# Performance work log

Measured on AMD Instinct MI355X. Metric: run time of the kernel, lower is better.

## Reference

```python
import jax, jax.numpy as jnp
import numpy as np

EPS = 1e-5
HEADS = 8
DIM_KEY = 128
K = 16           # num_experts_per_head
NUM_KEYS = 256   # sqrt(num_experts)


def setup_inputs() -> dict:
    key = jax.random.key(0)
    ks = jax.random.split(key, 5)
    B, T, D = 1, 1024, 1024
    x = jax.random.normal(ks[0], (B, T, D), dtype=jnp.float32)
    norm_w = jnp.ones((D,), dtype=jnp.float32)
    wq = jax.random.normal(ks[1], (D, DIM_KEY * HEADS * 2), dtype=jnp.float32) * 0.02
    keys = jax.random.normal(ks[2], (HEADS, NUM_KEYS, 2, DIM_KEY), dtype=jnp.float32) * 0.02
    expert_down = jax.random.normal(ks[3], (NUM_KEYS * NUM_KEYS, D), dtype=jnp.float32) * 0.02
    expert_up = jax.random.normal(ks[4], (NUM_KEYS * NUM_KEYS, D), dtype=jnp.float32) * 0.02
    return {"x": x, "norm_w": norm_w, "wq": wq, "keys": keys,
            "expert_down": expert_down, "expert_up": expert_up}


def reference(x, norm_w, wq, keys, expert_down, expert_up):
    B, T, D = x.shape
    # RMSNorm
    inv = jax.lax.rsqrt(jnp.mean(x * x, axis=-1, keepdims=True) + EPS)
    x_norm = x * inv * norm_w                                   # [B,T,D]
    # queries -> [B,T,H,2,dk]
    q = (x_norm @ wq).reshape(B, T, HEADS, 2, DIM_KEY)
    # similarity with product keys: sim[p] for each of the two sub-key sets
    sim = jnp.einsum('bthpd,hkpd->pbthk', q, keys)              # [2,B,T,H,NUM_KEYS]
    s1, i1 = jax.lax.top_k(sim[0], K)                           # [B,T,H,K]
    s2, i2 = jax.lax.top_k(sim[1], K)
    # cartesian product of the two top-k sets
    all_idx = (i1[..., :, None] * NUM_KEYS + i2[..., None, :]).reshape(B, T, HEADS, K * K)
    all_scores = (s1[..., :, None] + s2[..., None, :]).reshape(B, T, HEADS, K * K)
    final_scores, pk = jax.lax.top_k(all_scores, K)             # [B,T,H,K]
    final_idx = jnp.take_along_axis(all_idx, pk, axis=-1)       # [B,T,H,K]
    # gather expert vectors
    wd = expert_down[final_idx]                                 # [B,T,H,K,D]
    wu = expert_up[final_idx]                                   # [B,T,H,K,D]
    hidden = jnp.einsum('btd,bthkd->bthk', x_norm, wd)
    hidden = jax.nn.gelu(hidden, approximate=False)             # torch nn.GELU default = erf
    hidden = hidden * jax.nn.relu(final_scores)
    out = jnp.einsum('bthk,bthkd->btd', hidden, wu)             # [B,T,D]
    return out
```

## Files before the change

kernel.cpp:

```cpp
#include <hip/hip_runtime.h>
#include <hip/hip_bf16.h>
#include <math.h>

#define T_TOK   1024
#define D_MODEL 1024
#define H_HEADS 8
#define DKEY    128
#define NKEYS   256
#define TOPK    16
#define TPB     4

__device__ __forceinline__ float dot4(float4 a, float4 b){
  return a.x*b.x + a.y*b.y + a.z*b.z + a.w*b.w;
}

__global__ __launch_bounds__(256) void k_rmsnorm(const float* __restrict__ x,
                                                 const float* __restrict__ nw,
                                                 float* __restrict__ xn)
{
  const int t = blockIdx.x, tid = threadIdx.x;
  const float4 v = *(const float4*)(x + (size_t)t*D_MODEL + tid*4);
  float ss = dot4(v, v);
  #pragma unroll
  for (int m = 1; m < 64; m <<= 1) ss += __shfl_xor(ss, m, 64);
  __shared__ float part[4];
  const int lane = tid & 63, wid = tid >> 6;
  if (lane == 0) part[wid] = ss;
  __syncthreads();
  const float tot = part[0] + part[1] + part[2] + part[3];
  const float inv = rsqrtf(tot * (1.0f/(float)D_MODEL) + 1e-5f);
  const float4 w = *(const float4*)(nw + tid*4);
  float4 o;
  o.x = v.x*inv*w.x; o.y = v.y*inv*w.y; o.z = v.z*inv*w.z; o.w = v.w*inv*w.w;
  *(float4*)(xn + (size_t)t*D_MODEL + tid*4) = o;
}

#define TBM 64
#define TBN 64
#define TBK 16
__global__ __launch_bounds__(256) void k_qgemm(const float* __restrict__ A,
                                               const float* __restrict__ B,
                                               float* __restrict__ C)
{
  const int N = 2048, Kd = 1024;
  __shared__ float As[TBK][TBM+4];
  __shared__ float Bs[TBK][TBN+4];
  const int tid = threadIdx.x;
  const int row0 = blockIdx.y * TBM, col0 = blockIdx.x * TBN;
  const int ar = tid >> 2,  ac = (tid & 3) * 4;
  const int br = tid >> 4,  bc = (tid & 15) * 4;
  const int ty = tid >> 4,  tx = tid & 15;
  float acc[4][4] = {{0}};
  for (int k0 = 0; k0 < Kd; k0 += TBK){
    const float4 a = *(const float4*)(A + (size_t)(row0+ar)*Kd + k0 + ac);
    const float4 b = *(const float4*)(B + (size_t)(k0+br)*N + col0 + bc);
    As[ac+0][ar] = a.x; As[ac+1][ar] = a.y; As[ac+2][ar] = a.z; As[ac+3][ar] = a.w;
    *(float4*)&Bs[br][bc] = b;
    __syncthreads();
    #pragma unroll
    for (int kk = 0; kk < TBK; kk++){
      const float4 av = *(const float4*)&As[kk][ty*4];
      const float4 bv = *(const float4*)&Bs[kk][tx*4];
      acc[0][0] += av.x*bv.x; acc[0][1] += av.x*bv.y; acc[0][2] += av.x*bv.z; acc[0][3] += av.x*bv.w;
      acc[1][0] += av.y*bv.x; acc[1][1] += av.y*bv.y; acc[1][2] += av.y*bv.z; acc[1][3] += av.y*bv.w;
      acc[2][0] += av.z*bv.x; acc[2][1] += av.z*bv.y; acc[2][2] += av.z*bv.z; acc[2][3] += av.z*bv.w;
      acc[3][0] += av.w*bv.x; acc[3][1] += av.w*bv.y; acc[3][2] += av.w*bv.z; acc[3][3] += av.w*bv.w;
    }
    __syncthreads();
  }
  #pragma unroll
  for (int i = 0; i < 4; i++){
    float4 o; o.x = acc[i][0]; o.y = acc[i][1]; o.z = acc[i][2]; o.w = acc[i][3];
    *(float4*)(C + (size_t)(row0 + ty*4 + i)*N + col0 + tx*4) = o;
  }
}

__global__ __launch_bounds__(256) void k_simgemm(const float* __restrict__ Q,
                                                 const float* __restrict__ keys,
                                                 float* __restrict__ sims)
{
  const int hp = blockIdx.z;
  const int t0 = blockIdx.y * 64, kb0 = blockIdx.x * 64;
  const float* A = Q + (size_t)t0*2048 + (hp>>1)*256 + (hp&1)*128;
  const float* B = keys + ((size_t)((hp>>1)*NKEYS + kb0)*2 + (hp&1)) * DKEY;
  __shared__ float As[TBK][64+4];
  __shared__ float Bs[TBK][64+4];
  const int tid = threadIdx.x;
  const int ar = tid >> 2, ac = (tid & 3) * 4;
  const int ty = tid >> 4, tx = tid & 15;
  float acc[4][4] = {{0}};
  for (int kd = 0; kd < DKEY; kd += TBK){
    const float4 a = *(const float4*)(A + (size_t)ar*2048 + kd + ac);
    const float4 b = *(const float4*)(B + (size_t)ar*256  + kd + ac);
    As[ac+0][ar] = a.x; As[ac+1][ar] = a.y; As[ac+2][ar] = a.z; As[ac+3][ar] = a.w;
    Bs[ac+0][ar] = b.x; Bs[ac+1][ar] = b.y; Bs[ac+2][ar] = b.z; Bs[ac+3][ar] = b.w;
    __syncthreads();
    #pragma unroll
    for (int kk = 0; kk < TBK; kk++){
      const float4 av = *(const float4*)&As[kk][ty*4];
      const float4 bv = *(const float4*)&Bs[kk][tx*4];
      acc[0][0] += av.x*bv.x; acc[0][1] += av.x*bv.y; acc[0][2] += av.x*bv.z; acc[0][3] += av.x*bv.w;
      acc[1][0] += av.y*bv.x; acc[1][1] += av.y*bv.y; acc[1][2] += av.y*bv.z; acc[1][3] += av.y*bv.w;
      acc[2][0] += av.z*bv.x; acc[2][1] += av.z*bv.y; acc[2][2] += av.z*bv.z; acc[2][3] += av.z*bv.w;
      acc[3][0] += av.w*bv.x; acc[3][1] += av.w*bv.y; acc[3][2] += av.w*bv.z; acc[3][3] += av.w*bv.w;
    }
    __syncthreads();
  }
  float* Cb = sims + (size_t)t0*4096 + hp*256 + kb0;
  #pragma unroll
  for (int i = 0; i < 4; i++){
    float4 o; o.x = acc[i][0]; o.y = acc[i][1]; o.z = acc[i][2]; o.w = acc[i][3];
    *(float4*)(Cb + (size_t)(ty*4 + i)*4096 + tx*4) = o;
  }
}

__device__ __forceinline__ void wave_top16(float v[4], int lane, float* tvO, int* tiO)
{
  for (int r = 0; r < 16; r++){
    float bv = v[0]; int bj = 0;
    #pragma unroll
    for (int j = 1; j < 4; j++) if (v[j] > bv){ bv = v[j]; bj = j; }
    int bi = lane*4 + bj;
    #pragma unroll
    for (int m = 1; m < 64; m <<= 1){
      const float ov = __shfl_xor(bv, m, 64);
      const int   oi = __shfl_xor(bi, m, 64);
      if (ov > bv || (ov == bv && oi < bi)){ bv = ov; bi = oi; }
    }
    if (lane == 0){ tvO[r] = bv; tiO[r] = bi; }
    if ((bi >> 2) == lane) v[bi & 3] = -INFINITY;
  }
}

__global__ __launch_bounds__(256) void k_topk(const float* __restrict__ sims,
                                              int* __restrict__ fidxO,
                                              float* __restrict__ gateO)
{
  const int h  = blockIdx.x;
  const int t0 = blockIdx.y * TPB;
  const int tid = threadIdx.x;
  const int w = tid >> 6, lane = tid & 63;
  const int t = t0 + w;
  __shared__ float tv[TPB][2][TOPK];
  __shared__ int   ti[TPB][2][TOPK];

  float v0[4], v1[4];
  {
    const float4 a = *(const float4*)(sims + (size_t)t*4096 + (h*2+0)*256 + lane*4);
    const float4 b = *(const float4*)(sims + (size_t)t*4096 + (h*2+1)*256 + lane*4);
    v0[0]=a.x; v0[1]=a.y; v0[2]=a.z; v0[3]=a.w;
    v1[0]=b.x; v1[1]=b.y; v1[2]=b.z; v1[3]=b.w;
  }
  wave_top16(v0, lane, &tv[w][0][0], &ti[w][0][0]);
  wave_top16(v1, lane, &tv[w][1][0], &ti[w][1][0]);

  float cv[4];
  const int i0 = lane >> 2;
  #pragma unroll
  for (int j = 0; j < 4; j++)
    cv[j] = tv[w][0][i0] + tv[w][1][4*(lane & 3) + j];

  const size_t obase = (size_t)((t)*H_HEADS + h) * TOPK;
  for (int r = 0; r < 16; r++){
    float bv = cv[0]; int bj = 0;
    #pragma unroll
    for (int j = 1; j < 4; j++) if (cv[j] > bv){ bv = cv[j]; bj = j; }
    int bc = lane*4 + bj;
    #pragma unroll
    for (int m = 1; m < 64; m <<= 1){
      const float ov = __shfl_xor(bv, m, 64);
      const int   oc = __shfl_xor(bc, m, 64);
      if (ov > bv || (ov == bv && oc < bc)){ bv = ov; bc = oc; }
    }
    if (lane == 0){
      fidxO[obase + r] = ti[w][0][bc >> 4] * NKEYS + ti[w][1][bc & 15];
      gateO[obase + r] = bv > 0.0f ? bv : 0.0f;
    }
    if ((bc >> 2) == lane) cv[bc & 3] = -INFINITY;
  }
}

__global__ __launch_bounds__(256) void k_expert(const float* __restrict__ xn,
                                                const float* __restrict__ ed,
                                                const float* __restrict__ eu,
                                                const int* __restrict__ fidx,
                                                const float* __restrict__ gate,
                                                float* __restrict__ out)
{
  const int t = blockIdx.x, tid = threadIdx.x;
  const int lane = tid & 63, wid = tid >> 6;
  const float4 xv = *(const float4*)(xn + (size_t)t*D_MODEL + tid*4);
  float4 acc = {0.f, 0.f, 0.f, 0.f};
  __shared__ int   sidx[TOPK];
  __shared__ float wred[TOPK][4];
  __shared__ float coeff[TOPK];

  for (int h = 0; h < H_HEADS; ++h){
    const int base = (t*H_HEADS + h)*TOPK;
    if (tid < TOPK) sidx[tid] = fidx[base + tid];
    __syncthreads();

    {
      float4 wv[TOPK];
      #pragma unroll
      for (int k = 0; k < TOPK; k++)
        wv[k] = *(const float4*)(ed + (size_t)sidx[k]*D_MODEL + tid*4);
      #pragma unroll
      for (int k = 0; k < TOPK; k++){
        float p = dot4(xv, wv[k]);
        #pragma unroll
        for (int m = 1; m < 64; m <<= 1) p += __shfl_xor(p, m, 64);
        if (lane == 0) wred[k][wid] = p;
      }
    }
    __syncthreads();
    if (tid < TOPK){
      const float hsum = wred[tid][0] + wred[tid][1] + wred[tid][2] + wred[tid][3];
      const float g = 0.5f * hsum * (1.0f + erff(hsum * 0.70710678118654752440f));
      coeff[tid] = g * gate[base + tid];
    }
    __syncthreads();

    {
      float4 wv[TOPK];
      #pragma unroll
      for (int k = 0; k < TOPK; k++)
        wv[k] = *(const float4*)(eu + (size_t)sidx[k]*D_MODEL + tid*4);
      #pragma unroll
      for (int k = 0; k < TOPK; k++){
        const float c = coeff[k];
        acc.x += c*wv[k].x; acc.y += c*wv[k].y; acc.z += c*wv[k].z; acc.w += c*wv[k].w;
      }
    }
    __syncthreads();
  }
  *(float4*)(out + (size_t)t*D_MODEL + tid*4) = acc;
}

extern "C" void kernel_launch(void* const* d_in, const int* in_sizes, int n_in,
                              void* d_out, int out_size, void* d_ws, size_t ws_size,
                              hipStream_t stream)
{
  const float* x      = (const float*)d_in[0];
  const float* norm_w = (const float*)d_in[1];
  const float* wq     = (const float*)d_in[2];
  const float* keys   = (const float*)d_in[3];
  const float* ed     = (const float*)d_in[4];
  const float* eu     = (const float*)d_in[5];
  float* out = (float*)d_out;

  float* xn   = (float*)d_ws;
  float* q    = xn + (size_t)T_TOK * D_MODEL;
  int*   fidx = (int*)(q + (size_t)T_TOK * 2048);
  float* gate = (float*)(fidx + (size_t)T_TOK * H_HEADS * TOPK);
  float* sims = gate + (size_t)T_TOK * H_HEADS * TOPK;

  k_rmsnorm<<<T_TOK, 256, 0, stream>>>(x, norm_w, xn);
  k_qgemm<<<dim3(2048/TBN, 1024/TBM), 256, 0, stream>>>(xn, wq, q);
  k_simgemm<<<dim3(NKEYS/64, T_TOK/64, 16), 256, 0, stream>>>(q, keys, sims);
  k_topk<<<dim3(H_HEADS, T_TOK/TPB), 256, 0, stream>>>(sims, fidx, gate);
  k_expert<<<T_TOK, 256, 0, stream>>>(xn, ed, eu, fidx, gate, out);
}
```

Before: 321.0 us.

## Split expert stage into parallel down-projection and sync-free up-projection kernels

The fused per-token expert kernel, which looped over heads with several block barriers, is split into two kernels. The first launches one block per (token, head), with each wave computing four full-row dot products for the down projection, GELU and gate coefficients. The second accumulates all 128 up-projection rows per token with no per-head barriers, keeping 8 gathers in flight per step. This raises parallelism and memory-level concurrency for the gather-bound work, at the cost of an extra launch and a coefficient round-trip through global memory, which reuses the sims buffer.

```diff
diff --git a/kernel.cpp b/kernel.cpp
--- a/kernel.cpp
+++ b/kernel.cpp
@@ -180,59 +180,73 @@
   }
 }
 
-__global__ __launch_bounds__(256) void k_expert(const float* __restrict__ xn,
-                                                const float* __restrict__ ed,
-                                                const float* __restrict__ eu,
-                                                const int* __restrict__ fidx,
-                                                const float* __restrict__ gate,
-                                                float* __restrict__ out)
+__global__ __launch_bounds__(256) void k_peer_down(const float* __restrict__ xn,
+                                                   const float* __restrict__ ed,
+                                                   const int* __restrict__ fidx,
+                                                   const float* __restrict__ gate,
+                                                   float* __restrict__ coeff)
+{
+  const int b = blockIdx.x;
+  const int t = b >> 3;
+  const int tid = threadIdx.x, w = tid >> 6, lane = tid & 63;
+  const int base = b * TOPK;
+
+  float4 xv[4];
+  #pragma unroll
+  for (int j = 0; j < 4; j++)
+    xv[j] = *(const float4*)(xn + (size_t)t*D_MODEL + j*256 + lane*4);
+
+  int e[4];
+  #pragma unroll
+  for (int r = 0; r < 4; r++) e[r] = fidx[base + w*4 + r];
+
+  float4 wv[4][4];
+  #pragma unroll
+  for (int r = 0; r < 4; r++)
+    #pragma unroll
+    for (int j = 0; j < 4; j++)
+      wv[r][j] = *(const float4*)(ed + (size_t)e[r]*D_MODEL + j*256 + lane*4);
+
+  float s[4];
+  #pragma unroll
+  for (int r = 0; r < 4; r++){
+    float p = dot4(wv[r][0], xv[0]) + dot4(wv[r][1], xv[1])
+            + dot4(wv[r][2], xv[2]) + dot4(wv[r][3], xv[3]);
+    #pragma unroll
+    for (int m = 1; m < 64; m <<= 1) p += __shfl_xor(p, m, 64);
+    s[r] = p;
+  }
+  if (lane < 4){
+    const float hs = (lane == 0) ? s[0] : (lane == 1) ? s[1] : (lane == 2) ? s[2] : s[3];
+    const float g = 0.5f * hs * (1.0f + erff(hs * 0.70710678118654752440f));
+    coeff[base + w*4 + lane] = g * gate[base + w*4 + lane];
+  }
+}
+
+__global__ __launch_bounds__(256) void k_peer_up(const float* __restrict__ eu,
+                                                 const int* __restrict__ fidx,
+                                                 const float* __restrict__ coeff,
+                                                 float* __restrict__ out)
 {
   const int t = blockIdx.x, tid = threadIdx.x;
-  const int lane = tid & 63, wid = tid >> 6;
-  const float4 xv = *(const float4*)(xn + (size_t)t*D_MODEL + tid*4);
+  __shared__ int   sidx[H_HEADS*TOPK];
+  __shared__ float sc[H_HEADS*TOPK];
+  if (tid < H_HEADS*TOPK){
+    sidx[tid] = fidx[(size_t)t*H_HEADS*TOPK + tid];
+    sc[tid]   = coeff[(size_t)t*H_HEADS*TOPK + tid];
+  }
+  __syncthreads();
   float4 acc = {0.f, 0.f, 0.f, 0.f};
-  __shared__ int   sidx[TOPK];
-  __shared__ float wred[TOPK][4];
-  __shared__ float coeff[TOPK];
-
-  for (int h = 0; h < H_HEADS; ++h){
-    const int base = (t*H_HEADS + h)*TOPK;
-    if (tid < TOPK) sidx[tid] = fidx[base + tid];
-    __syncthreads();
-
-    {
-      float4 wv[TOPK];
-      #pragma unroll
-      for (int k = 0; k < TOPK; k++)
-        wv[k] = *(const float4*)(ed + (size_t)sidx[k]*D_MODEL + tid*4);
-      #pragma unroll
-      for (int k = 0; k < TOPK; k++){
-        float p = dot4(xv, wv[k]);
-        #pragma unroll
-        for (int m = 1; m < 64; m <<= 1) p += __shfl_xor(p, m, 64);
-        if (lane == 0) wred[k][wid] = p;
-      }
-    }
-    __syncthreads();
-    if (tid < TOPK){
-      const float hsum = wred[tid][0] + wred[tid][1] + wred[tid][2] + wred[tid][3];
-      const float g = 0.5f * hsum * (1.0f + erff(hsum * 0.70710678118654752440f));
-      coeff[tid] = g * gate[base + tid];
-    }
-    __syncthreads();
-
-    {
-      float4 wv[TOPK];
-      #pragma unroll
-      for (int k = 0; k < TOPK; k++)
-        wv[k] = *(const float4*)(eu + (size_t)sidx[k]*D_MODEL + tid*4);
-      #pragma unroll
-      for (int k = 0; k < TOPK; k++){
-        const float c = coeff[k];
-        acc.x += c*wv[k].x; acc.y += c*wv[k].y; acc.z += c*wv[k].z; acc.w += c*wv[k].w;
-      }
-    }
-    __syncthreads();
+  for (int j = 0; j < H_HEADS*TOPK; j += 8){
+    float4 wv[8];
+    #pragma unroll
+    for (int u = 0; u < 8; u++)
+      wv[u] = *(const float4*)(eu + (size_t)sidx[j+u]*D_MODEL + tid*4);
+    #pragma unroll
+    for (int u = 0; u < 8; u++){
+      const float c = sc[j+u];
+      acc.x += c*wv[u].x; acc.y += c*wv[u].y; acc.z += c*wv[u].z; acc.w += c*wv[u].w;
+    }
   }
   *(float4*)(out + (size_t)t*D_MODEL + tid*4) = acc;
 }
@@ -254,10 +268,12 @@
   int*   fidx = (int*)(q + (size_t)T_TOK * 2048);
   float* gate = (float*)(fidx + (size_t)T_TOK * H_HEADS * TOPK);
   float* sims = gate + (size_t)T_TOK * H_HEADS * TOPK;
+  float* coeff = sims;
 
   k_rmsnorm<<<T_TOK, 256, 0, stream>>>(x, norm_w, xn);
   k_qgemm<<<dim3(2048/TBN, 1024/TBM), 256, 0, stream>>>(xn, wq, q);
   k_simgemm<<<dim3(NKEYS/64, T_TOK/64, 16), 256, 0, stream>>>(q, keys, sims);
   k_topk<<<dim3(H_HEADS, T_TOK/TPB), 256, 0, stream>>>(sims, fidx, gate);
-  k_expert<<<T_TOK, 256, 0, stream>>>(xn, ed, eu, fidx, gate, out);
-}
+  k_peer_down<<<T_TOK*H_HEADS, 256, 0, stream>>>(xn, ed, fidx, gate, coeff);
+  k_peer_up<<<T_TOK, 256, 0, stream>>>(eu, fidx, coeff, out);
+}
```

Result: no change. 323.3 us (+0.7%).
